# Kernel optimization log

Hardware: AMD Instinct MI355X
Metric: run time of the kernel (lower is better)

Reference implementation:

```python
import jax, jax.numpy as jnp
import numpy as np

N_EMBD = 384
HEAD_SIZE = 64
B, T = 512, 256


def setup_inputs() -> dict:
    key = jax.random.key(0)
    ks = jax.random.split(key, 7)
    s = 1.0 / np.sqrt(N_EMBD)  # torch Linear default init scale
    return {
        "x": jax.random.normal(ks[0], (B, T, N_EMBD), dtype=jnp.float32),
        "Wq": jax.random.uniform(ks[1], (N_EMBD, HEAD_SIZE), jnp.float32, -s, s),
        "bq": jax.random.uniform(ks[2], (HEAD_SIZE,), jnp.float32, -s, s),
        "Wk": jax.random.uniform(ks[3], (N_EMBD, HEAD_SIZE), jnp.float32, -s, s),
        "bk": jax.random.uniform(ks[4], (HEAD_SIZE,), jnp.float32, -s, s),
        "Wv": jax.random.uniform(ks[5], (N_EMBD, HEAD_SIZE), jnp.float32, -s, s),
        "bv": jax.random.uniform(ks[6], (HEAD_SIZE,), jnp.float32, -s, s),
    }


def reference(x, Wq, bq, Wk, bk, Wv, bv):
    # Single causal self-attention head (nanoGPT 'Head', eval mode: dropout = identity)
    q = x @ Wq + bq  # [B, T, H]
    k = x @ Wk + bk
    v = x @ Wv + bv
    Tq = x.shape[1]
    scale = x.shape[-1] ** -0.5  # NOTE: source scales by n_embd (C), not head_size
    wei = jnp.einsum("btd,bsd->bts", q, k) * scale  # [B, T, T]
    mask = jnp.tril(jnp.ones((Tq, Tq), dtype=bool))
    wei = jnp.where(mask, wei, -jnp.inf)
    wei = jax.nn.softmax(wei, axis=-1)
    return jnp.einsum("bts,bsd->btd", wei, v)  # [B, T, H]
```

## Files before the change

### kernel.cpp

```cpp
#include <hip/hip_runtime.h>
#include <hip/hip_bf16.h>


#define Bsz 512
#define Tt  256
#define Cc  384
#define Hh  64

typedef __attribute__((ext_vector_type(8))) short bf16x8;
typedef __attribute__((ext_vector_type(4))) float f32x4;

__device__ __forceinline__ unsigned short f2bf(float f) {
    unsigned int u = __float_as_uint(f);
    unsigned int r = (u + 0x7fffu + ((u >> 16) & 1u)) >> 16;
    return (unsigned short)r;
}
__device__ __forceinline__ float bf2f(unsigned short b) {
    return __uint_as_float(((unsigned int)b) << 16);
}
__device__ __forceinline__ bf16x8 pack8v(f32x4 a, f32x4 b) {
    union { __hip_bfloat162 h2[4]; bf16x8 v; } u;
    u.h2[0] = __float22bfloat162_rn(float2{a[0], a[1]});
    u.h2[1] = __float22bfloat162_rn(float2{a[2], a[3]});
    u.h2[2] = __float22bfloat162_rn(float2{b[0], b[1]});
    u.h2[3] = __float22bfloat162_rn(float2{b[2], b[3]});
    return u.v;
}
__device__ __forceinline__ void gload_lds16(const void* g, void* l) {
    __builtin_amdgcn_global_load_lds(
        (const __attribute__((address_space(1))) unsigned int*)g,
        (__attribute__((address_space(3))) unsigned int*)l, 16, 0, 0);
}

__global__ __launch_bounds__(256) void prep_kernel(const float* __restrict__ Wq,
                                                   const float* __restrict__ Wk,
                                                   const float* __restrict__ Wv,
                                                   unsigned short* __restrict__ wtf) {
    int idx = blockIdx.x * 256 + threadIdx.x;
    if (idx >= 192 * 384) return;
    int j = idx & 7;
    int l = (idx >> 3) & 63;
    int t = idx >> 9;
    int kc = t / 12, nt = t - kc * 12;
    int n = nt * 16 + (l & 15);
    int k = kc * 32 + (l >> 4) * 8 + j;
    const float* W = (n < 64) ? Wq : ((n < 128) ? Wk : Wv);
    wtf[idx] = f2bf(W[k * 64 + (n & 63)]);
}

__global__ __launch_bounds__(1024, 4) void fused_kernel(
        const float* __restrict__ x,
        const float* __restrict__ bq,
        const float* __restrict__ bk,
        const float* __restrict__ bv,
        const unsigned short* __restrict__ wtf,
        float* __restrict__ out) {
    __shared__ unsigned short kl[16384];
    __shared__ unsigned short vl[16384];
    __shared__ unsigned short ql[16384];
    __shared__ unsigned short wtl[2][6144];

    const int tid = threadIdx.x;
    const int w = tid >> 6, lane = tid & 63, quad = lane >> 4, cl = lane & 15;
    const int wr = w & 7, wc = w >> 3;
    const int rb = blockIdx.x * 256;

    f32x4 acc[2][6];
#pragma unroll
    for (int rt = 0; rt < 2; ++rt)
#pragma unroll
        for (int nt = 0; nt < 6; ++nt) acc[rt][nt] = (f32x4){0.f, 0.f, 0.f, 0.f};

    const float* xp0 = x + (size_t)(rb + wr * 32 + cl) * Cc + quad * 8;
    const float* xp1 = xp0 + (size_t)16 * Cc;
    const bool dostage = tid < 768;
    const unsigned short* wsrc = wtf + tid * 8;
    unsigned short* wdst0 = &wtl[0][tid * 8];
    unsigned short* wdst1 = &wtl[1][tid * 8];

    if (dostage) gload_lds16(wsrc, wdst0);
    f32x4 A0 = *(const f32x4*)(xp0);
    f32x4 A1 = *(const f32x4*)(xp0 + 4);
    f32x4 A2 = *(const f32x4*)(xp1);
    f32x4 A3 = *(const f32x4*)(xp1 + 4);
    f32x4 B0, B1, B2, B3;

#define QKV_COMPUTE(BUF, X0, X1, X2, X3)                                             \
    {                                                                                \
        bf16x8 a0 = pack8v(X0, X1), a1 = pack8v(X2, X3);                             \
        _Pragma("unroll")                                                            \
        for (int nt = 0; nt < 6; ++nt) {                                             \
            bf16x8 bfr = *(const bf16x8*)&wtl[BUF][((wc * 6 + nt) * 64 + lane) * 8]; \
            acc[0][nt] = __builtin_amdgcn_mfma_f32_16x16x32_bf16(a0, bfr, acc[0][nt], 0, 0, 0); \
            acc[1][nt] = __builtin_amdgcn_mfma_f32_16x16x32_bf16(a1, bfr, acc[1][nt], 0, 0, 0); \
        }                                                                            \
    }

    for (int t = 0; t < 6; ++t) {
        const int kc = 2 * t;
        __syncthreads();
        if (dostage) gload_lds16(wsrc + (size_t)(kc + 1) * 6144, wdst1);
        B0 = *(const f32x4*)(xp0 + (kc + 1) * 32);
        B1 = *(const f32x4*)(xp0 + (kc + 1) * 32 + 4);
        B2 = *(const f32x4*)(xp1 + (kc + 1) * 32);
        B3 = *(const f32x4*)(xp1 + (kc + 1) * 32 + 4);
        QKV_COMPUTE(0, A0, A1, A2, A3)
        __syncthreads();
        if (t < 5) {
            if (dostage) gload_lds16(wsrc + (size_t)(kc + 2) * 6144, wdst0);
            A0 = *(const f32x4*)(xp0 + (kc + 2) * 32);
            A1 = *(const f32x4*)(xp0 + (kc + 2) * 32 + 4);
            A2 = *(const f32x4*)(xp1 + (kc + 2) * 32);
            A3 = *(const f32x4*)(xp1 + (kc + 2) * 32 + 4);
        }
        QKV_COMPUTE(1, B0, B1, B2, B3)
    }

#pragma unroll
    for (int nt = 0; nt < 6; ++nt) {
        const int colbase = wc * 96 + nt * 16;
        const int col = colbase + cl;
        if (colbase < 64) {
            float bias = bq[col];
            int sh = col >> 5, qp = (col >> 3) & 3, j = col & 7;
#pragma unroll
            for (int rt = 0; rt < 2; ++rt) {
                int m0 = wr * 32 + rt * 16 + quad * 4;
                int basei = (m0 >> 4) * 1024 + sh * 512 + qp * 128 + quad * 32 + j;
#pragma unroll
                for (int r = 0; r < 4; ++r)
                    ql[basei + r * 8] = f2bf(acc[rt][nt][r] + bias);
            }
        } else if (colbase < 128) {
            int h = col - 64;
            float bias = bk[h];
            int sh = h >> 5, qp = (h >> 3) & 3, j = h & 7;
#pragma unroll
            for (int rt = 0; rt < 2; ++rt) {
                int m0 = wr * 32 + rt * 16 + quad * 4;
                int basei = (m0 >> 4) * 1024 + sh * 512 + qp * 128 + quad * 32 + j;
#pragma unroll
                for (int r = 0; r < 4; ++r)
                    kl[basei + r * 8] = f2bf(acc[rt][nt][r] + bias);
            }
        } else {
            int h = col - 128;
            float bias = bv[h];
            int ht = h >> 4;
#pragma unroll
            for (int rt = 0; rt < 2; ++rt) {
                int m0 = wr * 32 + rt * 16 + quad * 4;
                int ks2 = m0 >> 5, qp = (m0 >> 3) & 3, j0 = m0 & 7;
                unsigned long long pk =
                      (unsigned long long)f2bf(acc[rt][nt][0] + bias)
                    | ((unsigned long long)f2bf(acc[rt][nt][1] + bias) << 16)
                    | ((unsigned long long)f2bf(acc[rt][nt][2] + bias) << 32)
                    | ((unsigned long long)f2bf(acc[rt][nt][3] + bias) << 48);
                *(unsigned long long*)&vl[(ks2 * 4 + ht) * 512 + qp * 128 + cl * 8 + j0] = pk;
            }
        }
    }
    __syncthreads();

    const float SL2E = 0.07362224f;
    unsigned short* P = &wtl[0][0] + w * 512;
    {
        const int W = w;
        const int qrow0 = W * 16;
        bf16x8 aq0 = *(const bf16x8*)&ql[(W * 128 + lane) * 8];
        bf16x8 aq1 = *(const bf16x8*)&ql[(W * 128 + 64 + lane) * 8];

        f32x4 o[4];
#pragma unroll
        for (int ht = 0; ht < 4; ++ht) o[ht] = (f32x4){0.f, 0.f, 0.f, 0.f};
        float rs[4] = {0.f, 0.f, 0.f, 0.f};

        const int nsteps = (qrow0 >> 5) + 1;
        for (int st = 0; st < nsteps; ++st) {
#pragma unroll
            for (int half = 0; half < 2; ++half) {
                int ct = st * 2 + half;
                bf16x8 b0 = *(const bf16x8*)&kl[(ct * 128 + lane) * 8];
                bf16x8 b1 = *(const bf16x8*)&kl[(ct * 128 + 64 + lane) * 8];
                f32x4 sc = (f32x4){0.f, 0.f, 0.f, 0.f};
                sc = __builtin_amdgcn_mfma_f32_16x16x32_bf16(aq0, b0, sc, 0, 0, 0);
                sc = __builtin_amdgcn_mfma_f32_16x16x32_bf16(aq1, b1, sc, 0, 0, 0);
                int key = ct * 16 + cl;
#pragma unroll
                for (int r = 0; r < 4; ++r) {
                    int row = quad * 4 + r;
                    float p = (key <= qrow0 + row) ? exp2f(sc[r] * SL2E) : 0.f;
                    unsigned short pb = f2bf(p);
                    rs[r] += bf2f(pb);
                    int k32 = half * 16 + cl;
                    int chunk = (k32 >> 3) ^ quad;
                    P[row * 32 + chunk * 8 + (k32 & 7)] = pb;
                }
            }
            bf16x8 bvf[4];
#pragma unroll
            for (int ht = 0; ht < 4; ++ht)
                bvf[ht] = *(const bf16x8*)&vl[((st * 4 + ht) * 64 + lane) * 8];

            asm volatile("s_waitcnt lgkmcnt(0)" ::: "memory");
            bf16x8 ap = *(const bf16x8*)((const char*)P + cl * 64 + ((quad ^ (cl >> 2)) & 3) * 16);
#pragma unroll
            for (int ht = 0; ht < 4; ++ht)
                o[ht] = __builtin_amdgcn_mfma_f32_16x16x32_bf16(ap, bvf[ht], o[ht], 0, 0, 0);
        }

#pragma unroll
        for (int r = 0; r < 4; ++r) {
            float s = rs[r];
            s += __shfl_xor(s, 1);
            s += __shfl_xor(s, 2);
            s += __shfl_xor(s, 4);
            s += __shfl_xor(s, 8);
            float inv = 1.0f / s;
            int t = qrow0 + quad * 4 + r;
#pragma unroll
            for (int ht = 0; ht < 4; ++ht)
                out[((size_t)(blockIdx.x * Tt + t)) * Hh + ht * 16 + cl] = o[ht][r] * inv;
        }
    }
}

extern "C" void kernel_launch(void* const* d_in, const int* in_sizes, int n_in,
                              void* d_out, int out_size, void* d_ws, size_t ws_size,
                              hipStream_t stream) {
    const float* x  = (const float*)d_in[0];
    const float* Wq = (const float*)d_in[1];
    const float* bq = (const float*)d_in[2];
    const float* Wk = (const float*)d_in[3];
    const float* bk = (const float*)d_in[4];
    const float* Wv = (const float*)d_in[5];
    const float* bv = (const float*)d_in[6];
    float* out = (float*)d_out;

    unsigned short* wtf = (unsigned short*)d_ws;

    prep_kernel<<<288, 256, 0, stream>>>(Wq, Wk, Wv, wtf);
    fused_kernel<<<Bsz, 1024, 0, stream>>>(x, bq, bk, bv, wtf, out);
}
```

Measured before the change: 323.1 us.

## Process two batches per block, overlapping attention of one with QKV projection of next

Each block now handles two batch elements with 512 threads (8 waves) instead of one with 1024. The attention phase for the first batch is interleaved slot-by-slot with the QKV projection MFMA loop for the second batch, so the two phases overlap. Each wave handles two query tiles (w and 15-w) to balance causal work. This adds register pressure (12x2 accumulators plus attention state) and relies on the correct LDS ordering of shared ql/kl/vl buffers between the phases.

```diff
diff --git a/kernel.cpp b/kernel.cpp
--- a/kernel.cpp
+++ b/kernel.cpp
@@ -48,180 +48,220 @@
     wtf[idx] = f2bf(W[k * 64 + (n & 63)]);
 }
 
-__global__ __launch_bounds__(1024, 4) void fused_kernel(
+__global__ __launch_bounds__(512, 2) void fused_kernel(
         const float* __restrict__ x,
         const float* __restrict__ bq,
         const float* __restrict__ bk,
         const float* __restrict__ bv,
         const unsigned short* __restrict__ wtf,
         float* __restrict__ out) {
+    __shared__ unsigned short ql[16384];
     __shared__ unsigned short kl[16384];
     __shared__ unsigned short vl[16384];
-    __shared__ unsigned short ql[16384];
     __shared__ unsigned short wtl[2][6144];
+    __shared__ unsigned short Pl[8 * 512];
 
     const int tid = threadIdx.x;
     const int w = tid >> 6, lane = tid & 63, quad = lane >> 4, cl = lane & 15;
-    const int wr = w & 7, wc = w >> 3;
-    const int rb = blockIdx.x * 256;
-
-    f32x4 acc[2][6];
-#pragma unroll
-    for (int rt = 0; rt < 2; ++rt)
-#pragma unroll
-        for (int nt = 0; nt < 6; ++nt) acc[rt][nt] = (f32x4){0.f, 0.f, 0.f, 0.f};
-
-    const float* xp0 = x + (size_t)(rb + wr * 32 + cl) * Cc + quad * 8;
-    const float* xp1 = xp0 + (size_t)16 * Cc;
-    const bool dostage = tid < 768;
-    const unsigned short* wsrc = wtf + tid * 8;
-    unsigned short* wdst0 = &wtl[0][tid * 8];
-    unsigned short* wdst1 = &wtl[1][tid * 8];
-
-    if (dostage) gload_lds16(wsrc, wdst0);
-    f32x4 A0 = *(const f32x4*)(xp0);
-    f32x4 A1 = *(const f32x4*)(xp0 + 4);
-    f32x4 A2 = *(const f32x4*)(xp1);
-    f32x4 A3 = *(const f32x4*)(xp1 + 4);
-    f32x4 B0, B1, B2, B3;
-
-#define QKV_COMPUTE(BUF, X0, X1, X2, X3)                                             \
-    {                                                                                \
-        bf16x8 a0 = pack8v(X0, X1), a1 = pack8v(X2, X3);                             \
+    const int bA = blockIdx.x * 2, bB = bA + 1;
+    const float SL2E = 0.07362224f;
+    unsigned short* Pw = &Pl[w * 512];
+
+    f32x4 acc[2][12];
+    f32x4 Xc0, Xc1, Xc2, Xc3, Xn0, Xn1, Xn2, Xn3;
+    int at_ti, at_W, at_qrow0, at_nsteps, at_st;
+    bf16x8 at_aq0, at_aq1;
+    f32x4 at_o[4];
+    float at_rs[4];
+
+#define ZERO_ACC()                                                                   \
+    _Pragma("unroll")                                                                \
+    for (int rt = 0; rt < 2; ++rt)                                                   \
         _Pragma("unroll")                                                            \
-        for (int nt = 0; nt < 6; ++nt) {                                             \
-            bf16x8 bfr = *(const bf16x8*)&wtl[BUF][((wc * 6 + nt) * 64 + lane) * 8]; \
-            acc[0][nt] = __builtin_amdgcn_mfma_f32_16x16x32_bf16(a0, bfr, acc[0][nt], 0, 0, 0); \
-            acc[1][nt] = __builtin_amdgcn_mfma_f32_16x16x32_bf16(a1, bfr, acc[1][nt], 0, 0, 0); \
+        for (int nt = 0; nt < 12; ++nt) acc[rt][nt] = (f32x4){0.f, 0.f, 0.f, 0.f};
+
+#define STAGE_W(c_) {                                                                \
+    const unsigned short* s_ = wtf + (size_t)(c_) * 6144;                            \
+    unsigned short* d_ = &wtl[(c_) & 1][0];                                          \
+    gload_lds16(s_ + tid * 8, d_ + tid * 8);                                         \
+    if (tid < 256) gload_lds16(s_ + (512 + tid) * 8, d_ + (512 + tid) * 8); }
+
+#define XLOAD(Xa, Xb, Xcc, Xd, xp0_, xp1_, k_)                                       \
+    Xa = *(const f32x4*)((xp0_) + (k_) * 32);                                        \
+    Xb = *(const f32x4*)((xp0_) + (k_) * 32 + 4);                                    \
+    Xcc = *(const f32x4*)((xp1_) + (k_) * 32);                                       \
+    Xd = *(const f32x4*)((xp1_) + (k_) * 32 + 4);
+
+#define QKV_MFMA(k_) {                                                               \
+    bf16x8 a0 = pack8v(Xc0, Xc1), a1 = pack8v(Xc2, Xc3);                             \
+    const unsigned short* wb = &wtl[(k_) & 1][0];                                    \
+    _Pragma("unroll")                                                                \
+    for (int nt = 0; nt < 12; ++nt) {                                                \
+        bf16x8 bfr = *(const bf16x8*)&wb[(nt * 64 + lane) * 8];                      \
+        acc[0][nt] = __builtin_amdgcn_mfma_f32_16x16x32_bf16(a0, bfr, acc[0][nt], 0, 0, 0); \
+        acc[1][nt] = __builtin_amdgcn_mfma_f32_16x16x32_bf16(a1, bfr, acc[1][nt], 0, 0, 0); \
+    } }
+
+#define EPILOGUE()                                                                   \
+    _Pragma("unroll")                                                                \
+    for (int nt = 0; nt < 12; ++nt) {                                                \
+        const int col = nt * 16 + cl;                                                \
+        if (nt < 4) {                                                                \
+            float bias = bq[col];                                                    \
+            int sh = col >> 5, qp = (col >> 3) & 3, j = col & 7;                     \
+            _Pragma("unroll")                                                        \
+            for (int rt = 0; rt < 2; ++rt) {                                         \
+                int m0 = w * 32 + rt * 16 + quad * 4;                                \
+                int basei = (m0 >> 4) * 1024 + sh * 512 + qp * 128 + quad * 32 + j;  \
+                _Pragma("unroll")                                                    \
+                for (int r = 0; r < 4; ++r)                                          \
+                    ql[basei + r * 8] = f2bf(acc[rt][nt][r] + bias);                 \
+            }                                                                        \
+        } else if (nt < 8) {                                                         \
+            int h = col - 64;                                                        \
+            float bias = bk[h];                                                      \
+            int sh = h >> 5, qp = (h >> 3) & 3, j = h & 7;                           \
+            _Pragma("unroll")                                                        \
+            for (int rt = 0; rt < 2; ++rt) {                                         \
+                int m0 = w * 32 + rt * 16 + quad * 4;                                \
+                int basei = (m0 >> 4) * 1024 + sh * 512 + qp * 128 + quad * 32 + j;  \
+                _Pragma("unroll")                                                    \
+                for (int r = 0; r < 4; ++r)                                          \
+                    kl[basei + r * 8] = f2bf(acc[rt][nt][r] + bias);                 \
+            }                                                                        \
+        } else {                                                                     \
+            int h = col - 128;                                                       \
+            float bias = bv[h];                                                      \
+            int ht = nt - 8;                                                         \
+            _Pragma("unroll")                                                        \
+            for (int rt = 0; rt < 2; ++rt) {                                         \
+                int m0 = w * 32 + rt * 16 + quad * 4;                                \
+                int ks2 = m0 >> 5, qp = (m0 >> 3) & 3, j0 = m0 & 7;                  \
+                unsigned long long pk =                                              \
+                      (unsigned long long)f2bf(acc[rt][nt][0] + bias)                \
+                    | ((unsigned long long)f2bf(acc[rt][nt][1] + bias) << 16)        \
+                    | ((unsigned long long)f2bf(acc[rt][nt][2] + bias) << 32)        \
+                    | ((unsigned long long)f2bf(acc[rt][nt][3] + bias) << 48);       \
+                *(unsigned long long*)&vl[(ks2 * 4 + ht) * 512 + qp * 128 + cl * 8 + j0] = pk; \
+            }                                                                        \
         }                                                                            \
     }
 
-    for (int t = 0; t < 6; ++t) {
-        const int kc = 2 * t;
-        __syncthreads();
-        if (dostage) gload_lds16(wsrc + (size_t)(kc + 1) * 6144, wdst1);
-        B0 = *(const f32x4*)(xp0 + (kc + 1) * 32);
-        B1 = *(const f32x4*)(xp0 + (kc + 1) * 32 + 4);
-        B2 = *(const f32x4*)(xp1 + (kc + 1) * 32);
-        B3 = *(const f32x4*)(xp1 + (kc + 1) * 32 + 4);
-        QKV_COMPUTE(0, A0, A1, A2, A3)
-        __syncthreads();
-        if (t < 5) {
-            if (dostage) gload_lds16(wsrc + (size_t)(kc + 2) * 6144, wdst0);
-            A0 = *(const f32x4*)(xp0 + (kc + 2) * 32);
-            A1 = *(const f32x4*)(xp0 + (kc + 2) * 32 + 4);
-            A2 = *(const f32x4*)(xp1 + (kc + 2) * 32);
-            A3 = *(const f32x4*)(xp1 + (kc + 2) * 32 + 4);
+#define ATT_INIT()                                                                   \
+    at_ti = 0; at_W = w; at_qrow0 = w * 16; at_nsteps = (w >> 1) + 1; at_st = 0;     \
+    at_aq0 = *(const bf16x8*)&ql[(at_W * 128 + lane) * 8];                           \
+    at_aq1 = *(const bf16x8*)&ql[(at_W * 128 + 64 + lane) * 8];                      \
+    at_o[0] = at_o[1] = at_o[2] = at_o[3] = (f32x4){0.f, 0.f, 0.f, 0.f};             \
+    at_rs[0] = at_rs[1] = at_rs[2] = at_rs[3] = 0.f;
+
+#define ATT_SLOT(bb)                                                                 \
+    if (at_ti < 2) {                                                                 \
+        if (at_st < at_nsteps) {                                                     \
+            const int st = at_st;                                                    \
+            _Pragma("unroll")                                                        \
+            for (int half = 0; half < 2; ++half) {                                   \
+                int ct = st * 2 + half;                                              \
+                bf16x8 b0 = *(const bf16x8*)&kl[(ct * 128 + lane) * 8];              \
+                bf16x8 b1 = *(const bf16x8*)&kl[(ct * 128 + 64 + lane) * 8];         \
+                f32x4 sc = (f32x4){0.f, 0.f, 0.f, 0.f};                              \
+                sc = __builtin_amdgcn_mfma_f32_16x16x32_bf16(at_aq0, b0, sc, 0, 0, 0); \
+                sc = __builtin_amdgcn_mfma_f32_16x16x32_bf16(at_aq1, b1, sc, 0, 0, 0); \
+                int key = ct * 16 + cl;                                              \
+                _Pragma("unroll")                                                    \
+                for (int r = 0; r < 4; ++r) {                                        \
+                    int row = quad * 4 + r;                                          \
+                    float p = (key <= at_qrow0 + row) ? exp2f(sc[r] * SL2E) : 0.f;   \
+                    unsigned short pb = f2bf(p);                                     \
+                    at_rs[r] += bf2f(pb);                                            \
+                    int k32 = half * 16 + cl;                                        \
+                    int chunk = (k32 >> 3) ^ quad;                                   \
+                    Pw[row * 32 + chunk * 8 + (k32 & 7)] = pb;                       \
+                }                                                                    \
+            }                                                                        \
+            bf16x8 bvf0 = *(const bf16x8*)&vl[((st * 4 + 0) * 64 + lane) * 8];       \
+            bf16x8 bvf1 = *(const bf16x8*)&vl[((st * 4 + 1) * 64 + lane) * 8];       \
+            bf16x8 bvf2 = *(const bf16x8*)&vl[((st * 4 + 2) * 64 + lane) * 8];       \
+            bf16x8 bvf3 = *(const bf16x8*)&vl[((st * 4 + 3) * 64 + lane) * 8];       \
+            asm volatile("s_waitcnt lgkmcnt(0)" ::: "memory");                       \
+            bf16x8 ap = *(const bf16x8*)((const char*)Pw + cl * 64 + ((quad ^ (cl >> 2)) & 3) * 16); \
+            at_o[0] = __builtin_amdgcn_mfma_f32_16x16x32_bf16(ap, bvf0, at_o[0], 0, 0, 0); \
+            at_o[1] = __builtin_amdgcn_mfma_f32_16x16x32_bf16(ap, bvf1, at_o[1], 0, 0, 0); \
+            at_o[2] = __builtin_amdgcn_mfma_f32_16x16x32_bf16(ap, bvf2, at_o[2], 0, 0, 0); \
+            at_o[3] = __builtin_amdgcn_mfma_f32_16x16x32_bf16(ap, bvf3, at_o[3], 0, 0, 0); \
+            ++at_st;                                                                 \
+        } else {                                                                     \
+            _Pragma("unroll")                                                        \
+            for (int r = 0; r < 4; ++r) {                                            \
+                float s = at_rs[r];                                                  \
+                s += __shfl_xor(s, 1);                                               \
+                s += __shfl_xor(s, 2);                                               \
+                s += __shfl_xor(s, 4);                                               \
+                s += __shfl_xor(s, 8);                                               \
+                float inv = 1.0f / s;                                                \
+                int t = at_qrow0 + quad * 4 + r;                                     \
+                _Pragma("unroll")                                                    \
+                for (int ht = 0; ht < 4; ++ht)                                       \
+                    out[((size_t)((bb) * Tt + t)) * Hh + ht * 16 + cl] = at_o[ht][r] * inv; \
+            }                                                                        \
+            ++at_ti;                                                                 \
+            if (at_ti == 1) {                                                        \
+                at_W = 15 - w; at_qrow0 = at_W * 16;                                 \
+                at_nsteps = (at_W >> 1) + 1; at_st = 0;                              \
+                at_aq0 = *(const bf16x8*)&ql[(at_W * 128 + lane) * 8];               \
+                at_aq1 = *(const bf16x8*)&ql[(at_W * 128 + 64 + lane) * 8];          \
+                at_o[0] = at_o[1] = at_o[2] = at_o[3] = (f32x4){0.f, 0.f, 0.f, 0.f}; \
+                at_rs[0] = at_rs[1] = at_rs[2] = at_rs[3] = 0.f;                     \
+            }                                                                        \
+        }                                                                            \
+    }
+
+    ZERO_ACC();
+    {
+        const float* xp0 = x + ((size_t)bA * 256 + w * 32 + cl) * Cc + quad * 8;
+        const float* xp1 = xp0 + 16 * Cc;
+        STAGE_W(0);
+        XLOAD(Xc0, Xc1, Xc2, Xc3, xp0, xp1, 0);
+#pragma unroll 1
+        for (int k = 0; k < 12; ++k) {
+            __syncthreads();
+            if (k < 11) {
+                STAGE_W(k + 1);
+                XLOAD(Xn0, Xn1, Xn2, Xn3, xp0, xp1, k + 1);
+            }
+            QKV_MFMA(k);
+            Xc0 = Xn0; Xc1 = Xn1; Xc2 = Xn2; Xc3 = Xn3;
         }
-        QKV_COMPUTE(1, B0, B1, B2, B3)
-    }
-
-#pragma unroll
-    for (int nt = 0; nt < 6; ++nt) {
-        const int colbase = wc * 96 + nt * 16;
-        const int col = colbase + cl;
-        if (colbase < 64) {
-            float bias = bq[col];
-            int sh = col >> 5, qp = (col >> 3) & 3, j = col & 7;
-#pragma unroll
-            for (int rt = 0; rt < 2; ++rt) {
-                int m0 = wr * 32 + rt * 16 + quad * 4;
-                int basei = (m0 >> 4) * 1024 + sh * 512 + qp * 128 + quad * 32 + j;
-#pragma unroll
-                for (int r = 0; r < 4; ++r)
-                    ql[basei + r * 8] = f2bf(acc[rt][nt][r] + bias);
-            }
-        } else if (colbase < 128) {
-            int h = col - 64;
-            float bias = bk[h];
-            int sh = h >> 5, qp = (h >> 3) & 3, j = h & 7;
-#pragma unroll
-            for (int rt = 0; rt < 2; ++rt) {
-                int m0 = wr * 32 + rt * 16 + quad * 4;
-                int basei = (m0 >> 4) * 1024 + sh * 512 + qp * 128 + quad * 32 + j;
-#pragma unroll
-                for (int r = 0; r < 4; ++r)
-                    kl[basei + r * 8] = f2bf(acc[rt][nt][r] + bias);
-            }
-        } else {
-            int h = col - 128;
-            float bias = bv[h];
-            int ht = h >> 4;
-#pragma unroll
-            for (int rt = 0; rt < 2; ++rt) {
-                int m0 = wr * 32 + rt * 16 + quad * 4;
-                int ks2 = m0 >> 5, qp = (m0 >> 3) & 3, j0 = m0 & 7;
-                unsigned long long pk =
-                      (unsigned long long)f2bf(acc[rt][nt][0] + bias)
-                    | ((unsigned long long)f2bf(acc[rt][nt][1] + bias) << 16)
-                    | ((unsigned long long)f2bf(acc[rt][nt][2] + bias) << 32)
-                    | ((unsigned long long)f2bf(acc[rt][nt][3] + bias) << 48);
-                *(unsigned long long*)&vl[(ks2 * 4 + ht) * 512 + qp * 128 + cl * 8 + j0] = pk;
-            }
+    }
+
+    const float* xpB0 = x + ((size_t)bB * 256 + w * 32 + cl) * Cc + quad * 8;
+    const float* xpB1 = xpB0 + 16 * Cc;
+    STAGE_W(0);
+    XLOAD(Xc0, Xc1, Xc2, Xc3, xpB0, xpB1, 0);
+
+    EPILOGUE();
+    ZERO_ACC();
+    __syncthreads();
+
+    ATT_INIT();
+#pragma unroll 1
+    for (int k = 0; k < 12; ++k) {
+        if (k) __syncthreads();
+        if (k < 11) {
+            STAGE_W(k + 1);
+            XLOAD(Xn0, Xn1, Xn2, Xn3, xpB0, xpB1, k + 1);
         }
-    }
+        ATT_SLOT(bA);
+        QKV_MFMA(k);
+        Xc0 = Xn0; Xc1 = Xn1; Xc2 = Xn2; Xc3 = Xn3;
+    }
+
+    EPILOGUE();
     __syncthreads();
 
-    const float SL2E = 0.07362224f;
-    unsigned short* P = &wtl[0][0] + w * 512;
-    {
-        const int W = w;
-        const int qrow0 = W * 16;
-        bf16x8 aq0 = *(const bf16x8*)&ql[(W * 128 + lane) * 8];
-        bf16x8 aq1 = *(const bf16x8*)&ql[(W * 128 + 64 + lane) * 8];
-
-        f32x4 o[4];
-#pragma unroll
-        for (int ht = 0; ht < 4; ++ht) o[ht] = (f32x4){0.f, 0.f, 0.f, 0.f};
-        float rs[4] = {0.f, 0.f, 0.f, 0.f};
-
-        const int nsteps = (qrow0 >> 5) + 1;
-        for (int st = 0; st < nsteps; ++st) {
-#pragma unroll
-            for (int half = 0; half < 2; ++half) {
-                int ct = st * 2 + half;
-                bf16x8 b0 = *(const bf16x8*)&kl[(ct * 128 + lane) * 8];
-                bf16x8 b1 = *(const bf16x8*)&kl[(ct * 128 + 64 + lane) * 8];
-                f32x4 sc = (f32x4){0.f, 0.f, 0.f, 0.f};
-                sc = __builtin_amdgcn_mfma_f32_16x16x32_bf16(aq0, b0, sc, 0, 0, 0);
-                sc = __builtin_amdgcn_mfma_f32_16x16x32_bf16(aq1, b1, sc, 0, 0, 0);
-                int key = ct * 16 + cl;
-#pragma unroll
-                for (int r = 0; r < 4; ++r) {
-                    int row = quad * 4 + r;
-                    float p = (key <= qrow0 + row) ? exp2f(sc[r] * SL2E) : 0.f;
-                    unsigned short pb = f2bf(p);
-                    rs[r] += bf2f(pb);
-                    int k32 = half * 16 + cl;
-                    int chunk = (k32 >> 3) ^ quad;
-                    P[row * 32 + chunk * 8 + (k32 & 7)] = pb;
-                }
-            }
-            bf16x8 bvf[4];
-#pragma unroll
-            for (int ht = 0; ht < 4; ++ht)
-                bvf[ht] = *(const bf16x8*)&vl[((st * 4 + ht) * 64 + lane) * 8];
-
-            asm volatile("s_waitcnt lgkmcnt(0)" ::: "memory");
-            bf16x8 ap = *(const bf16x8*)((const char*)P + cl * 64 + ((quad ^ (cl >> 2)) & 3) * 16);
-#pragma unroll
-            for (int ht = 0; ht < 4; ++ht)
-                o[ht] = __builtin_amdgcn_mfma_f32_16x16x32_bf16(ap, bvf[ht], o[ht], 0, 0, 0);
-        }
-
-#pragma unroll
-        for (int r = 0; r < 4; ++r) {
-            float s = rs[r];
-            s += __shfl_xor(s, 1);
-            s += __shfl_xor(s, 2);
-            s += __shfl_xor(s, 4);
-            s += __shfl_xor(s, 8);
-            float inv = 1.0f / s;
-            int t = qrow0 + quad * 4 + r;
-#pragma unroll
-            for (int ht = 0; ht < 4; ++ht)
-                out[((size_t)(blockIdx.x * Tt + t)) * Hh + ht * 16 + cl] = o[ht][r] * inv;
-        }
+    ATT_INIT();
+#pragma unroll 1
+    for (int sl = 0; sl < 11; ++sl) {
+        ATT_SLOT(bB);
     }
 }
 
@@ -240,5 +280,5 @@
     unsigned short* wtf = (unsigned short*)d_ws;
 
     prep_kernel<<<288, 256, 0, stream>>>(Wq, Wk, Wv, wtf);
-    fused_kernel<<<Bsz, 1024, 0, stream>>>(x, bq, bk, bv, wtf, out);
-}
+    fused_kernel<<<256, 512, 0, stream>>>(x, bq, bk, bv, wtf, out);
+}
```

New measurement: 314.5 us. 2.7% less time.
